# Optimization experiments

Measured on AMD Instinct MI355X. Metric: run time of the kernel, lower is better.

## Reference

```python
import jax, jax.numpy as jnp
import numpy as np

N, C, T, V = 128, 64, 128, 25   # batch, channels (in==out), frames, joints
R = 8                            # rel_channels = in_channels // rel_reduction
H = 12                           # SE hidden dim for joint attention (~V//2)


def setup_inputs() -> dict:
    key = jax.random.key(0)
    ks = jax.random.split(key, 8)
    w = lambda shape, k: jax.random.normal(k, shape, jnp.float32) * 0.05
    return {
        "x": jax.random.normal(ks[0], (N, C, T, V), jnp.float32),
        "A": jax.random.normal(ks[1], (V, V), jnp.float32) * 0.1,
        "w1": w((R, C), ks[2]), "b1": jnp.zeros((R,), jnp.float32),
        "w2": w((R, C), ks[3]), "b2": jnp.zeros((R,), jnp.float32),
        "w4": w((C, R), ks[4]), "b4": jnp.zeros((C,), jnp.float32),
        "se_w1": w((H, V), ks[5]), "se_b1": jnp.zeros((H,), jnp.float32),
        "se_w2": w((V, H), ks[6]), "se_b2": jnp.zeros((V,), jnp.float32),
    }


def reference(x, A, w1, b1, w2, b2, w4, b4, se_w1, se_b1, se_w2, se_b2):
    alpha = 1.0
    # conv1/conv2 are 1x1 convs; mean over T commutes with the linear map,
    # so pool first then project (saves a (N,R,T,V) intermediate).
    xm = x.mean(axis=2)                                     # (N,C,V)
    x1 = jnp.einsum('rc,ncv->nrv', w1, xm) + b1[None, :, None]
    x2 = jnp.einsum('rc,ncv->nrv', w2, xm) + b2[None, :, None]
    # channel-wise relation: broadcast diff + tanh  -> (N,R,V,V)
    rel = jnp.tanh(x1[:, :, :, None] - x2[:, :, None, :])
    # conv4 (1x1) lifts R->C, scale by alpha, add static adjacency
    Adyn = jnp.einsum('or,nruv->nouv', w4, rel) + b4[None, :, None, None]
    Adyn = Adyn * alpha + A[None, None]                     # (N,C,V,V)
    # DRJointSpa: SE attention over joints (pool C,T -> FC -> ReLU -> FC -> sigmoid)
    s = x.mean(axis=(1, 2))                                 # (N,V)
    h = jax.nn.relu(jnp.einsum('hv,nv->nh', se_w1, s) + se_b1)
    a = jax.nn.sigmoid(jnp.einsum('vh,nh->nv', se_w2, h) + se_b2)
    x3 = x * a[:, None, None, :]                            # (N,C,T,V)
    # per-channel graph aggregation over joints
    return jnp.einsum('ncuv,nctv->nctu', Adyn, x3)
```

## Files before the change

kernel.cpp:

```cpp
#include <hip/hip_runtime.h>
#include <hip/hip_bf16.h>

#define NN 128
#define CC 64
#define TT 128
#define VV 25
#define RR 8
#define HH 12
#define RELP 28
#define RELR (VV*RELP)
#define RELN (RR*RELR)
#define KP 40

typedef __attribute__((ext_vector_type(8))) short short8;
typedef __attribute__((ext_vector_type(4))) float f32x4;

__global__ __launch_bounds__(256) void kA_tmean(const float* __restrict__ x,
                                                float* __restrict__ xm) {
    const int blk = blockIdx.x;
    const int tid = threadIdx.x;
    __shared__ float st[TT * VV];
    __shared__ float ps[8 * VV];

    const float4* xb4 = (const float4*)(x + (size_t)blk * (TT * VV));
    float4* st4 = (float4*)st;
    for (int i = tid; i < (TT * VV) / 4; i += 256) st4[i] = xb4[i];
    __syncthreads();

    if (tid < 200) {
        const int v = tid % VV, tseg = tid / VV;
        float s = 0.f;
        const int base = tseg * 16 * VV + v;
#pragma unroll
        for (int i = 0; i < 16; i++) s += st[base + i * VV];
        ps[tseg * VV + v] = s;
    }
    __syncthreads();
    if (tid < VV) {
        float s = 0.f;
#pragma unroll
        for (int k = 0; k < 8; k++) s += ps[k * VV + tid];
        xm[(size_t)blk * VV + tid] = s * (1.f / TT);
    }
}

__global__ __launch_bounds__(256) void kB_small(
    const float* __restrict__ xm,
    const float* __restrict__ w1, const float* __restrict__ b1,
    const float* __restrict__ w2, const float* __restrict__ b2,
    const float* __restrict__ sw1, const float* __restrict__ sb1,
    const float* __restrict__ sw2, const float* __restrict__ sb2,
    float* __restrict__ a_out, float* __restrict__ rel_out) {
    const int n = blockIdx.x;
    const int tid = threadIdx.x;
    __shared__ float lxm[CC * VV];
    __shared__ float ls[VV];
    __shared__ float lh[HH];
    __shared__ float l1[RR * VV];
    __shared__ float l2[RR * VV];

    for (int i = tid; i < CC * VV; i += 256) lxm[i] = xm[(size_t)n * CC * VV + i];
    __syncthreads();

    if (tid < VV) {
        float s = 0.f;
        for (int c = 0; c < CC; c++) s += lxm[c * VV + tid];
        ls[tid] = s * (1.f / CC);
    }
    if (tid < RR * VV) {
        int r = tid / VV, v = tid % VV;
        float s1 = b1[r], s2 = b2[r];
        for (int c = 0; c < CC; c++) {
            float xv = lxm[c * VV + v];
            s1 += w1[r * CC + c] * xv;
            s2 += w2[r * CC + c] * xv;
        }
        l1[tid] = s1;
        l2[tid] = s2;
    }
    __syncthreads();

    if (tid < HH) {
        float h = sb1[tid];
        for (int v = 0; v < VV; v++) h += sw1[tid * VV + v] * ls[v];
        lh[tid] = fmaxf(h, 0.f);
    }
    __syncthreads();

    if (tid < VV) {
        float z = sb2[tid];
        for (int j = 0; j < HH; j++) z += sw2[tid * HH + j] * lh[j];
        a_out[(size_t)n * VV + tid] = 1.f / (1.f + expf(-z));
    }

    for (int idx = tid; idx < RELN; idx += 256) {
        int r = idx / RELR;
        int rem = idx - r * RELR;
        int u = rem / RELP;
        int v = rem - u * RELP;
        float val = 0.f;
        if (v < VV) val = tanhf(l1[r * VV + u] - l2[r * VV + v]);
        rel_out[(size_t)n * RELN + idx] = val;
    }
}

__global__ __launch_bounds__(256) void kC_main(
    const float* __restrict__ x, const float* __restrict__ A,
    const float* __restrict__ w4, const float* __restrict__ b4,
    const float* __restrict__ rel, const float* __restrict__ av,
    float* __restrict__ out) {
    const int blk = blockIdx.x;
    const int n = blk >> 6;
    const int c = blk & (CC - 1);
    const int tid = threadIdx.x;

    __shared__ __align__(16) unsigned short xsb[2][TT * KP];
    __shared__ __align__(16) unsigned short adb[2][32 * KP];
    float* os = (float*)&xsb[0][0];

    const float* xg = x + (size_t)blk * (TT * VV);

    {
        int t = tid / 13;
        int p = tid - t * 13;
#pragma unroll
        for (int it = 0; it < 7; ++it) {
            if (it < 6 || t < TT) {
                const float* row = xg + t * VV + 2 * p;
                float f0 = row[0];
                float f1 = row[(p < 12) ? 1 : 0];
                if (p >= 12) f1 = 0.f;
                unsigned int u0 = __builtin_bit_cast(unsigned int, f0);
                unsigned int u1 = __builtin_bit_cast(unsigned int, f1);
                unsigned int hb0 = u0 & 0xFFFF0000u;
                unsigned int hb1 = u1 & 0xFFFF0000u;
                float r0 = f0 - __builtin_bit_cast(float, hb0);
                float r1 = f1 - __builtin_bit_cast(float, hb1);
                unsigned int ru0 = __builtin_bit_cast(unsigned int, r0);
                unsigned int ru1 = __builtin_bit_cast(unsigned int, r1);
                *(unsigned int*)&xsb[0][t * KP + 2 * p] = (u0 >> 16) | hb1;
                *(unsigned int*)&xsb[1][t * KP + 2 * p] = (ru0 >> 16) | (ru1 & 0xFFFF0000u);
            }
            p += 9; t += 19;
            if (p >= 13) { p -= 13; ++t; }
        }
        for (int i = tid; i < TT * 3; i += 256) {
            int tt = i / 3, q = i - (i / 3) * 3;
            *(unsigned int*)&xsb[0][tt * KP + 26 + 2 * q] = 0u;
            *(unsigned int*)&xsb[1][tt * KP + 26 + 2 * q] = 0u;
        }
    }

    {
        float w4r[RR];
#pragma unroll
        for (int r = 0; r < RR; r++) w4r[r] = w4[c * RR + r];
        const float b4c = b4[c];

        if (tid < VV * 7) {
            const int u = tid / 7;
            const int v0 = (tid - u * 7) * 4;
            const float* rp = rel + (size_t)n * RELN + u * RELP + v0;
            float s0 = b4c, s1 = b4c, s2 = b4c, s3 = b4c;
#pragma unroll
            for (int r = 0; r < RR; r++) {
                const float4 rq = *(const float4*)(rp + r * RELR);
                s0 += w4r[r] * rq.x;
                s1 += w4r[r] * rq.y;
                s2 += w4r[r] * rq.z;
                s3 += w4r[r] * rq.w;
            }
            const int c0 = v0;
            const int c1 = min(v0 + 1, VV - 1);
            const int c2 = min(v0 + 2, VV - 1);
            const int c3 = min(v0 + 3, VV - 1);
            const float* Ar = A + u * VV;
            const float* avp = av + (size_t)n * VV;
            float o0 = (s0 + Ar[c0]) * avp[c0];
            float o1 = (s1 + Ar[c1]) * avp[c1];
            float o2 = (s2 + Ar[c2]) * avp[c2];
            float o3 = (s3 + Ar[c3]) * avp[c3];
            unsigned int u0 = __builtin_bit_cast(unsigned int, o0);
            unsigned int u1 = __builtin_bit_cast(unsigned int, o1);
            unsigned int u2 = __builtin_bit_cast(unsigned int, o2);
            unsigned int u3 = __builtin_bit_cast(unsigned int, o3);
            unsigned int hb0 = u0 & 0xFFFF0000u, hb1 = u1 & 0xFFFF0000u;
            unsigned int hb2 = u2 & 0xFFFF0000u, hb3 = u3 & 0xFFFF0000u;
            float r0 = o0 - __builtin_bit_cast(float, hb0);
            float r1 = o1 - __builtin_bit_cast(float, hb1);
            float r2 = o2 - __builtin_bit_cast(float, hb2);
            float r3 = o3 - __builtin_bit_cast(float, hb3);
            unsigned int ru0 = __builtin_bit_cast(unsigned int, r0);
            unsigned int ru1 = __builtin_bit_cast(unsigned int, r1);
            unsigned int ru2 = __builtin_bit_cast(unsigned int, r2);
            unsigned int ru3 = __builtin_bit_cast(unsigned int, r3);
            *(unsigned int*)&adb[0][u * KP + v0]     = (u0 >> 16) | hb1;
            *(unsigned int*)&adb[0][u * KP + v0 + 2] = (u2 >> 16) | hb3;
            *(unsigned int*)&adb[1][u * KP + v0]     = (ru0 >> 16) | (ru1 & 0xFFFF0000u);
            *(unsigned int*)&adb[1][u * KP + v0 + 2] = (ru2 >> 16) | (ru3 & 0xFFFF0000u);
        }
        if (tid < 25 * 6) {
            int u = tid / 6, q = tid - (tid / 6) * 6;
            *(unsigned int*)&adb[0][u * KP + 28 + 2 * q] = 0u;
            *(unsigned int*)&adb[1][u * KP + 28 + 2 * q] = 0u;
        }
        for (int i = tid; i < 7 * 20; i += 256) {
            int rr2 = i / 20, cc2 = i - (i / 20) * 20;
            *(unsigned int*)&adb[0][(VV + rr2) * KP + 2 * cc2] = 0u;
            *(unsigned int*)&adb[1][(VV + rr2) * KP + 2 * cc2] = 0u;
        }
    }
    __syncthreads();

    const int wid = tid >> 6;
    const int lane = tid & 63;
    const int fr = lane & 15;
    const int fk = (lane >> 4) * 8;

    f32x4 acc[2][2] = {};
    short8 ah[2], al[2], bh[2], bl[2];
#pragma unroll
    for (int mi = 0; mi < 2; ++mi) {
        const int m = (wid * 2 + mi) * 16 + fr;
        ah[mi] = *(const short8*)&xsb[0][m * KP + fk];
        al[mi] = *(const short8*)&xsb[1][m * KP + fk];
    }
#pragma unroll
    for (int ni = 0; ni < 2; ++ni) {
        const int nn2 = ni * 16 + fr;
        bh[ni] = *(const short8*)&adb[0][nn2 * KP + fk];
        bl[ni] = *(const short8*)&adb[1][nn2 * KP + fk];
    }
#pragma unroll
    for (int mi = 0; mi < 2; ++mi)
#pragma unroll
        for (int ni = 0; ni < 2; ++ni) {
            acc[mi][ni] = __builtin_amdgcn_mfma_f32_16x16x32_bf16(ah[mi], bh[ni], acc[mi][ni], 0, 0, 0);
            acc[mi][ni] = __builtin_amdgcn_mfma_f32_16x16x32_bf16(ah[mi], bl[ni], acc[mi][ni], 0, 0, 0);
            acc[mi][ni] = __builtin_amdgcn_mfma_f32_16x16x32_bf16(al[mi], bh[ni], acc[mi][ni], 0, 0, 0);
        }
    __syncthreads();

#pragma unroll
    for (int mi = 0; mi < 2; ++mi) {
        const int tb = (wid * 2 + mi) * 16 + (lane >> 4) * 4;
#pragma unroll
        for (int ni = 0; ni < 2; ++ni) {
            const int u = ni * 16 + fr;
            if (u < VV) {
#pragma unroll
                for (int r = 0; r < 4; ++r)
                    os[(tb + r) * VV + u] = acc[mi][ni][r];
            }
        }
    }
    __syncthreads();

    float4* ob4 = (float4*)(out + (size_t)blk * (TT * VV));
    const float4* os4 = (const float4*)os;
    ob4[tid]       = os4[tid];
    ob4[tid + 256] = os4[tid + 256];
    ob4[tid + 512] = os4[tid + 512];
    if (tid < 32) ob4[tid + 768] = os4[tid + 768];
}

extern "C" void kernel_launch(void* const* d_in, const int* in_sizes, int n_in,
                              void* d_out, int out_size, void* d_ws, size_t ws_size,
                              hipStream_t stream) {
    const float* x   = (const float*)d_in[0];
    const float* A   = (const float*)d_in[1];
    const float* w1  = (const float*)d_in[2];
    const float* b1  = (const float*)d_in[3];
    const float* w2  = (const float*)d_in[4];
    const float* b2  = (const float*)d_in[5];
    const float* w4  = (const float*)d_in[6];
    const float* b4  = (const float*)d_in[7];
    const float* sw1 = (const float*)d_in[8];
    const float* sb1 = (const float*)d_in[9];
    const float* sw2 = (const float*)d_in[10];
    const float* sb2 = (const float*)d_in[11];
    float* out = (float*)d_out;

    float* ws = (float*)d_ws;
    float* xm  = ws;
    float* a_s = xm + (size_t)NN * CC * VV;
    float* rel = a_s + (size_t)NN * VV;

    kA_tmean<<<NN * CC, 256, 0, stream>>>(x, xm);
    kB_small<<<NN, 256, 0, stream>>>(xm, w1, b1, w2, b2, sw1, sb1, sw2, sb2, a_s, rel);
    kC_main<<<NN * CC, 256, 0, stream>>>(x, A, w4, b4, rel, a_s, out);
}
```

Baseline: 231.5 us.

## Load x tiles directly into MFMA register fragments, skipping LDS staging

The main kernel no longer stages x in shared memory as split bf16 hi/lo arrays. Each lane now loads its 8 contiguous floats straight from global memory into registers and converts them to hi/lo bf16 fragments in place, with lane group 3 handling the single leftover joint. This removes the LDS write/read round trip and one barrier, and frees shared memory. The output store becomes nontemporal. The trade-off is unaligned vector global loads and a different occupancy and LDS footprint.

```diff
diff --git a/kernel.cpp b/kernel.cpp
--- a/kernel.cpp
+++ b/kernel.cpp
@@ -14,6 +14,43 @@
 
 typedef __attribute__((ext_vector_type(8))) short short8;
 typedef __attribute__((ext_vector_type(4))) float f32x4;
+typedef __attribute__((ext_vector_type(4))) unsigned int u32x4;
+
+__device__ __forceinline__ void loadu8(const float* p, f32x4& a, f32x4& b) {
+    __builtin_memcpy(&a, p, 16);
+    __builtin_memcpy(&b, p + 4, 16);
+}
+
+__device__ __forceinline__ void cvt8(const f32x4& a, const f32x4& b,
+                                     short8& hi, short8& lo) {
+    float f[8] = {a.x, a.y, a.z, a.w, b.x, b.y, b.z, b.w};
+    unsigned int u[8], r[8];
+#pragma unroll
+    for (int j = 0; j < 8; j++) u[j] = __builtin_bit_cast(unsigned int, f[j]);
+#pragma unroll
+    for (int j = 0; j < 8; j++)
+        r[j] = __builtin_bit_cast(unsigned int,
+                 f[j] - __builtin_bit_cast(float, u[j] & 0xFFFF0000u));
+    u32x4 H = { (u[0] >> 16) | (u[1] & 0xFFFF0000u),
+                (u[2] >> 16) | (u[3] & 0xFFFF0000u),
+                (u[4] >> 16) | (u[5] & 0xFFFF0000u),
+                (u[6] >> 16) | (u[7] & 0xFFFF0000u) };
+    u32x4 L = { (r[0] >> 16) | (r[1] & 0xFFFF0000u),
+                (r[2] >> 16) | (r[3] & 0xFFFF0000u),
+                (r[4] >> 16) | (r[5] & 0xFFFF0000u),
+                (r[6] >> 16) | (r[7] & 0xFFFF0000u) };
+    hi = __builtin_bit_cast(short8, H);
+    lo = __builtin_bit_cast(short8, L);
+}
+
+__device__ __forceinline__ void cvt1(float s, short8& hi, short8& lo) {
+    unsigned int us = __builtin_bit_cast(unsigned int, s);
+    float rs = s - __builtin_bit_cast(float, us & 0xFFFF0000u);
+    u32x4 H = { us >> 16, 0u, 0u, 0u };
+    u32x4 L = { __builtin_bit_cast(unsigned int, rs) >> 16, 0u, 0u, 0u };
+    hi = __builtin_bit_cast(short8, H);
+    lo = __builtin_bit_cast(short8, L);
+}
 
 __global__ __launch_bounds__(256) void kA_tmean(const float* __restrict__ x,
                                                 float* __restrict__ xm) {
@@ -114,41 +151,27 @@
     const int c = blk & (CC - 1);
     const int tid = threadIdx.x;
 
-    __shared__ __align__(16) unsigned short xsb[2][TT * KP];
     __shared__ __align__(16) unsigned short adb[2][32 * KP];
-    float* os = (float*)&xsb[0][0];
+    __shared__ __align__(16) float os[TT * VV];
 
     const float* xg = x + (size_t)blk * (TT * VV);
 
-    {
-        int t = tid / 13;
-        int p = tid - t * 13;
-#pragma unroll
-        for (int it = 0; it < 7; ++it) {
-            if (it < 6 || t < TT) {
-                const float* row = xg + t * VV + 2 * p;
-                float f0 = row[0];
-                float f1 = row[(p < 12) ? 1 : 0];
-                if (p >= 12) f1 = 0.f;
-                unsigned int u0 = __builtin_bit_cast(unsigned int, f0);
-                unsigned int u1 = __builtin_bit_cast(unsigned int, f1);
-                unsigned int hb0 = u0 & 0xFFFF0000u;
-                unsigned int hb1 = u1 & 0xFFFF0000u;
-                float r0 = f0 - __builtin_bit_cast(float, hb0);
-                float r1 = f1 - __builtin_bit_cast(float, hb1);
-                unsigned int ru0 = __builtin_bit_cast(unsigned int, r0);
-                unsigned int ru1 = __builtin_bit_cast(unsigned int, r1);
-                *(unsigned int*)&xsb[0][t * KP + 2 * p] = (u0 >> 16) | hb1;
-                *(unsigned int*)&xsb[1][t * KP + 2 * p] = (ru0 >> 16) | (ru1 & 0xFFFF0000u);
-            }
-            p += 9; t += 19;
-            if (p >= 13) { p -= 13; ++t; }
-        }
-        for (int i = tid; i < TT * 3; i += 256) {
-            int tt = i / 3, q = i - (i / 3) * 3;
-            *(unsigned int*)&xsb[0][tt * KP + 26 + 2 * q] = 0u;
-            *(unsigned int*)&xsb[1][tt * KP + 26 + 2 * q] = 0u;
-        }
+    const int wid = tid >> 6;
+    const int lane = tid & 63;
+    const int fr = lane & 15;
+    const int fkq = lane >> 4;
+    const int fk = fkq * 8;
+    const int m0 = (wid * 2 + 0) * 16 + fr;
+    const int m1 = (wid * 2 + 1) * 16 + fr;
+
+    f32x4 qa00, qa01, qa10, qa11;
+    float qs0 = 0.f, qs1 = 0.f;
+    if (fkq < 3) {
+        loadu8(xg + m0 * VV + fk, qa00, qa01);
+        loadu8(xg + m1 * VV + fk, qa10, qa11);
+    } else {
+        qs0 = xg[m0 * VV + 24];
+        qs1 = xg[m1 * VV + 24];
     }
 
     {
@@ -204,46 +227,43 @@
             *(unsigned int*)&adb[0][u * KP + 28 + 2 * q] = 0u;
             *(unsigned int*)&adb[1][u * KP + 28 + 2 * q] = 0u;
         }
-        for (int i = tid; i < 7 * 20; i += 256) {
-            int rr2 = i / 20, cc2 = i - (i / 20) * 20;
+        if (tid < 7 * 20) {
+            int rr2 = tid / 20, cc2 = tid - (tid / 20) * 20;
             *(unsigned int*)&adb[0][(VV + rr2) * KP + 2 * cc2] = 0u;
             *(unsigned int*)&adb[1][(VV + rr2) * KP + 2 * cc2] = 0u;
         }
     }
     __syncthreads();
 
-    const int wid = tid >> 6;
-    const int lane = tid & 63;
-    const int fr = lane & 15;
-    const int fk = (lane >> 4) * 8;
-
-    f32x4 acc[2][2] = {};
-    short8 ah[2], al[2], bh[2], bl[2];
-#pragma unroll
-    for (int mi = 0; mi < 2; ++mi) {
-        const int m = (wid * 2 + mi) * 16 + fr;
-        ah[mi] = *(const short8*)&xsb[0][m * KP + fk];
-        al[mi] = *(const short8*)&xsb[1][m * KP + fk];
-    }
+    short8 ah0, al0, ah1, al1;
+    if (fkq < 3) {
+        cvt8(qa00, qa01, ah0, al0);
+        cvt8(qa10, qa11, ah1, al1);
+    } else {
+        cvt1(qs0, ah0, al0);
+        cvt1(qs1, ah1, al1);
+    }
+    short8 bh[2], bl[2];
 #pragma unroll
     for (int ni = 0; ni < 2; ++ni) {
         const int nn2 = ni * 16 + fr;
         bh[ni] = *(const short8*)&adb[0][nn2 * KP + fk];
         bl[ni] = *(const short8*)&adb[1][nn2 * KP + fk];
     }
-#pragma unroll
-    for (int mi = 0; mi < 2; ++mi)
-#pragma unroll
-        for (int ni = 0; ni < 2; ++ni) {
-            acc[mi][ni] = __builtin_amdgcn_mfma_f32_16x16x32_bf16(ah[mi], bh[ni], acc[mi][ni], 0, 0, 0);
-            acc[mi][ni] = __builtin_amdgcn_mfma_f32_16x16x32_bf16(ah[mi], bl[ni], acc[mi][ni], 0, 0, 0);
-            acc[mi][ni] = __builtin_amdgcn_mfma_f32_16x16x32_bf16(al[mi], bh[ni], acc[mi][ni], 0, 0, 0);
-        }
-    __syncthreads();
+    f32x4 acc[2][2] = {};
+#pragma unroll
+    for (int ni = 0; ni < 2; ++ni) {
+        acc[0][ni] = __builtin_amdgcn_mfma_f32_16x16x32_bf16(ah0, bh[ni], acc[0][ni], 0, 0, 0);
+        acc[0][ni] = __builtin_amdgcn_mfma_f32_16x16x32_bf16(ah0, bl[ni], acc[0][ni], 0, 0, 0);
+        acc[0][ni] = __builtin_amdgcn_mfma_f32_16x16x32_bf16(al0, bh[ni], acc[0][ni], 0, 0, 0);
+        acc[1][ni] = __builtin_amdgcn_mfma_f32_16x16x32_bf16(ah1, bh[ni], acc[1][ni], 0, 0, 0);
+        acc[1][ni] = __builtin_amdgcn_mfma_f32_16x16x32_bf16(ah1, bl[ni], acc[1][ni], 0, 0, 0);
+        acc[1][ni] = __builtin_amdgcn_mfma_f32_16x16x32_bf16(al1, bh[ni], acc[1][ni], 0, 0, 0);
+    }
 
 #pragma unroll
     for (int mi = 0; mi < 2; ++mi) {
-        const int tb = (wid * 2 + mi) * 16 + (lane >> 4) * 4;
+        const int tb = (wid * 2 + mi) * 16 + fkq * 4;
 #pragma unroll
         for (int ni = 0; ni < 2; ++ni) {
             const int u = ni * 16 + fr;
@@ -256,12 +276,12 @@
     }
     __syncthreads();
 
-    float4* ob4 = (float4*)(out + (size_t)blk * (TT * VV));
-    const float4* os4 = (const float4*)os;
-    ob4[tid]       = os4[tid];
-    ob4[tid + 256] = os4[tid + 256];
-    ob4[tid + 512] = os4[tid + 512];
-    if (tid < 32) ob4[tid + 768] = os4[tid + 768];
+    f32x4* ob4 = (f32x4*)(out + (size_t)blk * (TT * VV));
+    const f32x4* os4 = (const f32x4*)os;
+    __builtin_nontemporal_store(os4[tid],       &ob4[tid]);
+    __builtin_nontemporal_store(os4[tid + 256], &ob4[tid + 256]);
+    __builtin_nontemporal_store(os4[tid + 512], &ob4[tid + 512]);
+    if (tid < 32) __builtin_nontemporal_store(os4[tid + 768], &ob4[tid + 768]);
 }
 
 extern "C" void kernel_launch(void* const* d_in, const int* in_sizes, int n_in,
```

New measurement: 230.5 us. Within noise of the previous version (-0.4%).
